# Kernel optimization log

Measured on AMD Instinct MI355X. Metric: run time of the kernel, lower is better.

## Reference

```python
import jax, jax.numpy as jnp
import numpy as np

SCALE = 256.0
QMIN, QMAX = -32768.0, 32767.0
EPS = 1e-5
NUM_HEADS = 16

def fpq(t):
    return jnp.clip(jnp.round(t * SCALE), QMIN, QMAX) / SCALE

def layer_norm(x, g, b):
    mu = jnp.mean(x, axis=-1, keepdims=True)
    var = jnp.mean(jnp.square(x - mu), axis=-1, keepdims=True)
    return (x - mu) * jax.lax.rsqrt(var + EPS) * g + b

def setup_inputs() -> dict:
    key = jax.random.key(0)
    ks = jax.random.split(key, 10)
    B, S, D, H = 8, 1024, 1024, 4096
    s = 1.0 / np.sqrt(D)
    sh = 1.0 / np.sqrt(H)
    return {
        "x": jax.random.normal(ks[0], (B, S, D), jnp.float32),
        "Wqkv": jax.random.uniform(ks[1], (D, 3 * D), jnp.float32, -s, s),
        "bqkv": jax.random.uniform(ks[2], (3 * D,), jnp.float32, -s, s),
        "Wout": jax.random.uniform(ks[3], (D, D), jnp.float32, -s, s),
        "bout": jax.random.uniform(ks[4], (D,), jnp.float32, -s, s),
        "W1": jax.random.uniform(ks[5], (D, H), jnp.float32, -s, s),
        "b1": jax.random.uniform(ks[6], (H,), jnp.float32, -s, s),
        "W2": jax.random.uniform(ks[7], (H, D), jnp.float32, -sh, sh),
        "b2": jax.random.uniform(ks[8], (D,), jnp.float32, -sh, sh),
        "g1": jnp.ones((D,), jnp.float32),
        "beta1": jnp.zeros((D,), jnp.float32),
        "g2": jnp.ones((D,), jnp.float32),
        "beta2": jnp.zeros((D,), jnp.float32),
    }

def reference(x, Wqkv, bqkv, Wout, bout, W1, b1, W2, b2, g1, beta1, g2, beta2):
    B, S, D = x.shape
    Hh = NUM_HEADS
    hd = D // Hh
    # --- attention on norm1(x) ---
    xn = layer_norm(x, g1, beta1)
    qkv = fpq(xn @ Wqkv + bqkv)                       # [B,S,3D]
    q, k, v = jnp.split(qkv, 3, axis=-1)
    q = q.reshape(B, S, Hh, hd).transpose(0, 2, 1, 3)  # [B,H,S,hd]
    k = k.reshape(B, S, Hh, hd).transpose(0, 2, 1, 3)
    v = v.reshape(B, S, Hh, hd).transpose(0, 2, 1, 3)
    scores = jnp.einsum("bhqd,bhkd->bhqk", q, k) / np.sqrt(hd)
    probs = fpq(jax.nn.softmax(scores, axis=-1))
    ctx = jnp.einsum("bhqk,bhkd->bhqd", probs, v)
    ctx = ctx.transpose(0, 2, 1, 3).reshape(B, S, D)
    attn = fpq(ctx @ Wout + bout)
    x = fpq(x + fpq(attn))
    # --- MLP on norm2(x) ---
    xn2 = layer_norm(x, g2, beta2)
    h = jax.nn.relu(fpq(xn2 @ W1 + b1))
    mlp = fpq(h @ W2 + b2)
    x = fpq(x + fpq(mlp))
    return x
```

## Files before the change

### kernel.cpp

```cpp
#include <hip/hip_runtime.h>
#include <hip/hip_fp16.h>
#include <stdint.h>

typedef _Float16 f16;
typedef _Float16 f16x4 __attribute__((ext_vector_type(4)));
typedef _Float16 f16x8 __attribute__((ext_vector_type(8)));
typedef float f32x4 __attribute__((ext_vector_type(4)));

__device__ __forceinline__ float fpq(float t) {
    float r = rintf(t * 256.0f);
    r = fminf(fmaxf(r, -32768.0f), 32767.0f);
    return r * 0.00390625f;
}

__device__ __forceinline__ int swzkey(int r) { return (r & 3) | ((r >> 1) & 4); }

__device__ __forceinline__ void gll16(const f16* g, f16* l) {
    __builtin_amdgcn_global_load_lds(
        (const __attribute__((address_space(1))) uint32_t*)g,
        (__attribute__((address_space(3))) uint32_t*)l, 16, 0, 0);
}

template <int N> __device__ __forceinline__ void waitvm() {
    if constexpr (N == 0)      asm volatile("s_waitcnt vmcnt(0)" ::: "memory");
    else if constexpr (N == 1) asm volatile("s_waitcnt vmcnt(1)" ::: "memory");
    else if constexpr (N == 2) asm volatile("s_waitcnt vmcnt(2)" ::: "memory");
    else if constexpr (N == 4) asm volatile("s_waitcnt vmcnt(4)" ::: "memory");
    else if constexpr (N == 6) asm volatile("s_waitcnt vmcnt(6)" ::: "memory");
    else                       asm volatile("s_waitcnt vmcnt(8)" ::: "memory");
}

__global__ __launch_bounds__(256) void ln_kernel(
        const float* __restrict__ x, const float* __restrict__ g,
        const float* __restrict__ b, f16* __restrict__ out) {
    int row = blockIdx.x;
    int t = threadIdx.x;
    const float4* xr = (const float4*)(x + (size_t)row * 1024);
    float4 v = xr[t];
    float s = v.x + v.y + v.z + v.w;
    float s2 = v.x * v.x + v.y * v.y + v.z * v.z + v.w * v.w;
#pragma unroll
    for (int o = 32; o >= 1; o >>= 1) {
        s += __shfl_down(s, o);
        s2 += __shfl_down(s2, o);
    }
    __shared__ float red[8];
    int wid = t >> 6;
    if ((t & 63) == 0) { red[wid] = s; red[4 + wid] = s2; }
    __syncthreads();
    float ts = red[0] + red[1] + red[2] + red[3];
    float ts2 = red[4] + red[5] + red[6] + red[7];
    float mu = ts * (1.0f / 1024.0f);
    float var = ts2 * (1.0f / 1024.0f) - mu * mu;
    float rs = rsqrtf(var + 1e-5f);
    float4 gg = ((const float4*)g)[t];
    float4 bb = ((const float4*)b)[t];
    f16x4 o4;
    o4[0] = (f16)((v.x - mu) * rs * gg.x + bb.x);
    o4[1] = (f16)((v.y - mu) * rs * gg.y + bb.y);
    o4[2] = (f16)((v.z - mu) * rs * gg.z + bb.z);
    o4[3] = (f16)((v.w - mu) * rs * gg.w + bb.w);
    ((f16x4*)out)[(size_t)row * 256 + t] = o4;
}

__global__ __launch_bounds__(256) void transpose_kernel(
        const float* __restrict__ W, f16* __restrict__ WT, int K, int N) {
    __shared__ float tile[32][33];
    int n0 = blockIdx.x * 32, k0 = blockIdx.y * 32;
    int tx = threadIdx.x & 31, ty = threadIdx.x >> 5;
#pragma unroll
    for (int i = 0; i < 32; i += 8)
        tile[ty + i][tx] = W[(size_t)(k0 + ty + i) * N + n0 + tx];
    __syncthreads();
#pragma unroll
    for (int i = 0; i < 32; i += 8)
        WT[(size_t)(n0 + ty + i) * K + k0 + tx] = (f16)tile[tx][ty + i];
}

template <int EPI>
__global__ __launch_bounds__(256, 2) void gemmd_kernel(
        const f16* __restrict__ A, const f16* __restrict__ BT,
        int N, int K, int GM, int GN,
        const float* __restrict__ bias, const float* __restrict__ resid,
        void* __restrict__ out0, f16* __restrict__ outk, f16* __restrict__ outv) {
    constexpr int ABUF = 128 * 64;
    constexpr int BUFSZ = 2 * ABUF;
    __shared__ f16 lds[2 * BUFSZ];

    int nwg = GM * GN;
    int orig = blockIdx.x;
    int wg = (orig & 7) * (nwg >> 3) + (orig >> 3);
    int st = wg >> 6, in = wg & 63;
    int bm = (st % (GM >> 3)) * 8 + (in >> 3);
    int bn = (st / (GM >> 3)) * 8 + (in & 7);
    int m0 = bm * 128, n0 = bn * 128;
    int tid = threadIdx.x;
    int lane = tid & 63;
    int lr = lane & 15, lg = lane >> 4;
    int wv = tid >> 6;
    int wm = wv >> 1, wn = wv & 1;

    size_t srcA[4], srcB[4]; int dst[4];
#pragma unroll
    for (int j = 0; j < 4; ++j) {
        int row = j * 32 + (tid >> 3);
        int slot = (tid & 7) ^ (row & 7);
        srcA[j] = (size_t)(m0 + row) * K + slot * 8;
        srcB[j] = (size_t)(n0 + row) * K + slot * 8;
        dst[j] = j * 2048 + tid * 8;
    }

    int offA[2][4], offB[4][2];
#pragma unroll
    for (int i = 0; i < 4; ++i) {
        int row = wm * 64 + i * 16 + lr;
#pragma unroll
        for (int kk = 0; kk < 2; ++kk)
            offA[kk][i] = row * 64 + (((kk * 4 + lg) ^ (row & 7)) * 8);
    }
#pragma unroll
    for (int j = 0; j < 4; ++j) {
        int n = wn * 64 + j * 16 + lr;
#pragma unroll
        for (int kk = 0; kk < 2; ++kk)
            offB[j][kk] = ABUF + n * 64 + (((kk * 4 + lg) ^ (n & 7)) * 8);
    }

    f32x4 acc[4][4] = {};
    int NT = K >> 6;

#pragma unroll
    for (int j = 0; j < 4; ++j) gll16(A + srcA[j], lds + dst[j]);
#pragma unroll
    for (int j = 0; j < 4; ++j) gll16(BT + srcB[j], lds + ABUF + dst[j]);
#pragma unroll
    for (int j = 0; j < 4; ++j) gll16(A + srcA[j] + 64, lds + BUFSZ + dst[j]);
#pragma unroll
    for (int j = 0; j < 4; ++j) gll16(BT + srcB[j] + 64, lds + BUFSZ + ABUF + dst[j]);
    waitvm<8>();
    __builtin_amdgcn_s_barrier();
    __builtin_amdgcn_sched_barrier(0);

    for (int t = 0; t < NT; ++t) {
        int cur = t & 1;
        f16* Ab = lds + cur * BUFSZ;
        f16x8 a0[4], a1[4], b00, b01, b10, b11;
#pragma unroll
        for (int i = 0; i < 4; ++i) a0[i] = *(const f16x8*)&Ab[offA[0][i]];
        b00 = *(const f16x8*)&Ab[offB[0][0]];
        b01 = *(const f16x8*)&Ab[offB[1][0]];
#pragma unroll
        for (int i = 0; i < 4; ++i) a1[i] = *(const f16x8*)&Ab[offA[1][i]];
        b10 = *(const f16x8*)&Ab[offB[0][1]];
        b11 = *(const f16x8*)&Ab[offB[1][1]];
        __builtin_amdgcn_s_setprio(1);
#pragma unroll
        for (int i = 0; i < 4; ++i) {
            acc[i][0] = __builtin_amdgcn_mfma_f32_16x16x32_f16(a0[i], b00, acc[i][0], 0, 0, 0);
            acc[i][1] = __builtin_amdgcn_mfma_f32_16x16x32_f16(a0[i], b01, acc[i][1], 0, 0, 0);
        }
#pragma unroll
        for (int i = 0; i < 4; ++i) {
            acc[i][0] = __builtin_amdgcn_mfma_f32_16x16x32_f16(a1[i], b10, acc[i][0], 0, 0, 0);
            acc[i][1] = __builtin_amdgcn_mfma_f32_16x16x32_f16(a1[i], b11, acc[i][1], 0, 0, 0);
        }
        __builtin_amdgcn_s_setprio(0);
        f16x8 b20 = *(const f16x8*)&Ab[offB[2][0]];
        f16x8 b30 = *(const f16x8*)&Ab[offB[3][0]];
        f16x8 b21 = *(const f16x8*)&Ab[offB[2][1]];
        f16x8 b31 = *(const f16x8*)&Ab[offB[3][1]];
        asm volatile("s_waitcnt lgkmcnt(0)" ::: "memory");
        __builtin_amdgcn_sched_barrier(0);
        __builtin_amdgcn_s_barrier();
        if (t + 2 < NT) {
            size_t kof = (size_t)(t + 2) << 6;
#pragma unroll
            for (int j = 0; j < 4; ++j) gll16(A + srcA[j] + kof, Ab + dst[j]);
#pragma unroll
            for (int j = 0; j < 4; ++j) gll16(BT + srcB[j] + kof, Ab + ABUF + dst[j]);
        }
        __builtin_amdgcn_s_setprio(1);
#pragma unroll
        for (int i = 0; i < 4; ++i) {
            acc[i][2] = __builtin_amdgcn_mfma_f32_16x16x32_f16(a0[i], b20, acc[i][2], 0, 0, 0);
            acc[i][3] = __builtin_amdgcn_mfma_f32_16x16x32_f16(a0[i], b30, acc[i][3], 0, 0, 0);
        }
#pragma unroll
        for (int i = 0; i < 4; ++i) {
            acc[i][2] = __builtin_amdgcn_mfma_f32_16x16x32_f16(a1[i], b21, acc[i][2], 0, 0, 0);
            acc[i][3] = __builtin_amdgcn_mfma_f32_16x16x32_f16(a1[i], b31, acc[i][3], 0, 0, 0);
        }
        __builtin_amdgcn_s_setprio(0);
        if (t + 2 < NT) { waitvm<8>(); }
        else if (t + 1 < NT) { waitvm<0>(); }
        __builtin_amdgcn_sched_barrier(0);
        __builtin_amdgcn_s_barrier();
    }

#pragma unroll
    for (int i = 0; i < 4; ++i) {
#pragma unroll
        for (int j = 0; j < 4; ++j) {
            int col = n0 + wn * 64 + j * 16 + lr;
            float bv = bias[col];
#pragma unroll
            for (int r = 0; r < 4; ++r) {
                int row = m0 + wm * 64 + i * 16 + lg * 4 + r;
                float val = acc[i][j][r] + bv;
                if (EPI == 0) {
                    float qv = fpq(val);
                    int part = col >> 10, wi = col & 1023;
                    int hd = wi >> 6, d = wi & 63;
                    int bb = row >> 10, ss = row & 1023;
                    size_t bh = (size_t)(bb * 16 + hd);
                    if (part == 0) {
                        ((f16*)out0)[(bh * 1024 + ss) * 64 + d] = (f16)qv;
                    } else if (part == 1) {
                        outk[bh * 65536 + (ss >> 6) * 4096 + (ss & 63) * 64 + (d ^ (swzkey(ss) << 3))] = (f16)qv;
                    } else {
                        outv[bh * 65536 + (ss >> 6) * 4096 + d * 64 + ((ss & 63) ^ (swzkey(d) << 3))] = (f16)qv;
                    }
                } else if (EPI == 2) {
                    float hv = fmaxf(fpq(val), 0.0f);
                    ((f16*)out0)[(size_t)row * N + col] = (f16)hv;
                } else {
                    float o = fpq(resid[(size_t)row * 1024 + col] + fpq(val));
                    ((float*)out0)[(size_t)row * 1024 + col] = o;
                }
            }
        }
    }
}

__global__ __launch_bounds__(512) void attn_kernel(
        const f16* __restrict__ Q, const f16* __restrict__ Kg,
        const f16* __restrict__ Vt, f16* __restrict__ ctx) {
    int id = blockIdx.x;
    int qt = (id >> 3) & 7;
    int bh = (id >> 6) * 8 + (id & 7);
    int b = bh >> 4, h = bh & 15;
    const f16* Qp = Q + ((size_t)bh * 1024 + (size_t)qt * 128) * 64;
    const f16* Kp = Kg + (size_t)bh * 65536;
    const f16* Vp = Vt + (size_t)bh * 65536;
    int t = threadIdx.x, lane = t & 63, w = t >> 6;
    int lr = lane & 15, lg = lane >> 4;
    __shared__ f16 Ks[2][4096];
    __shared__ f16 Vs[2][4096];
    int so = t * 8;

    const float L2E = 1.4426950408889634f;
    const float C0 = -24.0f * 1.4426950408889634f;

    f16x8 qf[2];
#pragma unroll
    for (int kk = 0; kk < 2; ++kk) {
        qf[kk] = *(const f16x8*)(Qp + (w * 16 + lr) * 64 + kk * 32 + lg * 8);
#pragma unroll
        for (int j = 0; j < 8; ++j) qf[kk][j] = qf[kk][j] * (f16)0.125f;
    }
    int koff[4][2], voff[4][2];
#pragma unroll
    for (int nf = 0; nf < 4; ++nf) {
        int rowv = 32 * (nf >> 1) + 8 * ((lr >> 2) ^ (2 * (nf & 1))) + 4 * (nf & 1) + (lr & 3);
#pragma unroll
        for (int kk = 0; kk < 2; ++kk)
            koff[nf][kk] = rowv * 64 + (((kk * 4 + lg) ^ swzkey(rowv)) * 8);
    }
#pragma unroll
    for (int db = 0; db < 4; ++db) {
        int d = db * 16 + lr;
#pragma unroll
        for (int kk = 0; kk < 2; ++kk)
            voff[db][kk] = d * 64 + (((kk * 4 + lg) ^ swzkey(d)) * 8);
    }

    gll16(Kp + so, Ks[0] + so);
    float lsum = 0.0f;
    for (int kt = 0; kt < 16; ++kt) {
        int cur = kt & 1;
        if (kt < 15) {
            gll16(Kp + (kt + 1) * 4096 + so, Ks[cur ^ 1] + so);
            waitvm<1>();
        } else {
            waitvm<0>();
        }
        __builtin_amdgcn_sched_barrier(0);
        __builtin_amdgcn_s_barrier();
        f32x4 sc[4] = {};
#pragma unroll
        for (int kk = 0; kk < 2; ++kk)
#pragma unroll
            for (int nf = 0; nf < 4; ++nf) {
                f16x8 kf = *(const f16x8*)&Ks[cur][koff[nf][kk]];
                sc[nf] = __builtin_amdgcn_mfma_f32_16x16x32_f16(kf, qf[kk], sc[nf], 0, 0, 0);
            }
        float part = 0.0f;
#pragma unroll
        for (int nf = 0; nf < 4; ++nf)
#pragma unroll
            for (int r = 0; r < 4; ++r)
                part += __builtin_amdgcn_exp2f(fmaf(sc[nf][r], L2E, C0));
        lsum += part;
        __builtin_amdgcn_s_barrier();
    }
    lsum += __shfl_xor(lsum, 16);
    lsum += __shfl_xor(lsum, 32);
    float rl256 = 256.0f * __builtin_amdgcn_rcpf(lsum);

    f32x4 co[4] = {};
    const float inv256 = 0.00390625f;
    gll16(Kp + so, Ks[0] + so);
    gll16(Vp + so, Vs[0] + so);
    for (int kt = 0; kt < 16; ++kt) {
        int cur = kt & 1;
        if (kt < 15) {
            gll16(Kp + (kt + 1) * 4096 + so, Ks[cur ^ 1] + so);
            gll16(Vp + (kt + 1) * 4096 + so, Vs[cur ^ 1] + so);
            waitvm<2>();
        } else {
            waitvm<0>();
        }
        __builtin_amdgcn_sched_barrier(0);
        __builtin_amdgcn_s_barrier();
        f32x4 sc[4] = {};
#pragma unroll
        for (int kk = 0; kk < 2; ++kk)
#pragma unroll
            for (int nf = 0; nf < 4; ++nf) {
                f16x8 kf = *(const f16x8*)&Ks[cur][koff[nf][kk]];
                sc[nf] = __builtin_amdgcn_mfma_f32_16x16x32_f16(kf, qf[kk], sc[nf], 0, 0, 0);
            }
        uint32_t pk0[4], pk1[4];
#pragma unroll
        for (int nf = 0; nf < 4; ++nf) {
            float e0 = __builtin_amdgcn_exp2f(fmaf(sc[nf][0], L2E, C0));
            float e1 = __builtin_amdgcn_exp2f(fmaf(sc[nf][1], L2E, C0));
            float e2 = __builtin_amdgcn_exp2f(fmaf(sc[nf][2], L2E, C0));
            float e3 = __builtin_amdgcn_exp2f(fmaf(sc[nf][3], L2E, C0));
            float r0 = rintf(e0 * rl256);
            float r1 = rintf(e1 * rl256);
            float r2 = rintf(e2 * rl256);
            float r3 = rintf(e3 * rl256);
            pk0[nf] = __builtin_bit_cast(uint32_t,
                        __builtin_amdgcn_cvt_pkrtz(r0 * inv256, r1 * inv256));
            pk1[nf] = __builtin_bit_cast(uint32_t,
                        __builtin_amdgcn_cvt_pkrtz(r2 * inv256, r3 * inv256));
        }
#pragma unroll
        for (int kk = 0; kk < 2; ++kk) {
            uint4 fw;
            fw.x = pk0[2 * kk];
            fw.y = pk1[2 * kk];
            fw.z = __shfl_xor(pk0[2 * kk + 1], 32);
            fw.w = __shfl_xor(pk1[2 * kk + 1], 32);
            f16x8 pa = __builtin_bit_cast(f16x8, fw);
#pragma unroll
            for (int db = 0; db < 4; ++db) {
                f16x8 vb = *(const f16x8*)&Vs[cur][voff[db][kk]];
                co[db] = __builtin_amdgcn_mfma_f32_16x16x32_f16(pa, vb, co[db], 0, 0, 0);
            }
        }
        __builtin_amdgcn_s_barrier();
    }
#pragma unroll
    for (int db = 0; db < 4; ++db)
#pragma unroll
        for (int r = 0; r < 4; ++r) {
            int ss = qt * 128 + w * 16 + lg * 4 + r;
            ctx[((size_t)b * 1024 + ss) * 1024 + h * 64 + db * 16 + lr] = (f16)co[db][r];
        }
}

extern "C" void kernel_launch(void* const* d_in, const int* in_sizes, int n_in,
                              void* d_out, int out_size, void* d_ws, size_t ws_size,
                              hipStream_t stream) {
    const float* x     = (const float*)d_in[0];
    const float* Wqkv  = (const float*)d_in[1];
    const float* bqkv  = (const float*)d_in[2];
    const float* Wout  = (const float*)d_in[3];
    const float* bout  = (const float*)d_in[4];
    const float* W1    = (const float*)d_in[5];
    const float* b1    = (const float*)d_in[6];
    const float* W2    = (const float*)d_in[7];
    const float* b2    = (const float*)d_in[8];
    const float* g1    = (const float*)d_in[9];
    const float* beta1 = (const float*)d_in[10];
    const float* g2    = (const float*)d_in[11];
    const float* beta2 = (const float*)d_in[12];

    char* ws = (char*)d_ws;
    const size_t MB = 1ull << 20;
    f16*  q_h   = (f16*)(ws);
    f16*  k_h   = (f16*)(ws + 16 * MB);
    f16*  vt_h  = (f16*)(ws + 32 * MB);
    f16*  ctx_h = (f16*)(ws + 48 * MB);
    f16*  h_h   = (f16*)(ws);
    f16*  xn_h  = (f16*)(ws + 64 * MB);
    float* x1   = (float*)(ws + 80 * MB);
    f16*  wT    = (f16*)(ws + 112 * MB);

    ln_kernel<<<8192, 256, 0, stream>>>(x, g1, beta1, xn_h);
    transpose_kernel<<<dim3(96, 32), 256, 0, stream>>>(Wqkv, wT, 1024, 3072);
    gemmd_kernel<0><<<1536, 256, 0, stream>>>(xn_h, wT, 3072, 1024, 64, 24, bqkv, nullptr, q_h, k_h, vt_h);
    attn_kernel<<<1024, 512, 0, stream>>>(q_h, k_h, vt_h, ctx_h);
    transpose_kernel<<<dim3(32, 32), 256, 0, stream>>>(Wout, wT, 1024, 1024);
    gemmd_kernel<1><<<512, 256, 0, stream>>>(ctx_h, wT, 1024, 1024, 64, 8, bout, x, x1, nullptr, nullptr);
    ln_kernel<<<8192, 256, 0, stream>>>(x1, g2, beta2, xn_h);
    transpose_kernel<<<dim3(128, 32), 256, 0, stream>>>(W1, wT, 1024, 4096);
    gemmd_kernel<2><<<2048, 256, 0, stream>>>(xn_h, wT, 4096, 1024, 64, 32, b1, nullptr, h_h, nullptr, nullptr);
    transpose_kernel<<<dim3(32, 128), 256, 0, stream>>>(W2, wT, 4096, 1024);
    gemmd_kernel<3><<<512, 256, 0, stream>>>(h_h, wT, 1024, 4096, 64, 8, b2, x1, d_out, nullptr, nullptr);
}
```

Measured before the change: 364.0 us.

## Halve GEMM K-tile to 32 and raise occupancy to four workgroups per CU

```diff
diff --git a/kernel.cpp b/kernel.cpp
--- a/kernel.cpp
+++ b/kernel.cpp
@@ -14,6 +14,7 @@
 }
 
 __device__ __forceinline__ int swzkey(int r) { return (r & 3) | ((r >> 1) & 4); }
+__device__ __forceinline__ int kk2(int r) { return (r >> 1) & 3; }
 
 __device__ __forceinline__ void gll16(const f16* g, f16* l) {
     __builtin_amdgcn_global_load_lds(
@@ -78,12 +79,12 @@
 }
 
 template <int EPI>
-__global__ __launch_bounds__(256, 2) void gemmd_kernel(
+__global__ __launch_bounds__(256, 4) void gemmd_kernel(
         const f16* __restrict__ A, const f16* __restrict__ BT,
         int N, int K, int GM, int GN,
         const float* __restrict__ bias, const float* __restrict__ resid,
         void* __restrict__ out0, f16* __restrict__ outk, f16* __restrict__ outv) {
-    constexpr int ABUF = 128 * 64;
+    constexpr int ABUF = 128 * 32;
     constexpr int BUFSZ = 2 * ABUF;
     __shared__ f16 lds[2 * BUFSZ];
 
@@ -100,98 +101,65 @@
     int wv = tid >> 6;
     int wm = wv >> 1, wn = wv & 1;
 
-    size_t srcA[4], srcB[4]; int dst[4];
-#pragma unroll
-    for (int j = 0; j < 4; ++j) {
-        int row = j * 32 + (tid >> 3);
-        int slot = (tid & 7) ^ (row & 7);
+    size_t srcA[2], srcB[2]; int dst[2];
+#pragma unroll
+    for (int j = 0; j < 2; ++j) {
+        int row = j * 64 + (tid >> 2);
+        int slot = (tid & 3) ^ kk2(row);
         srcA[j] = (size_t)(m0 + row) * K + slot * 8;
         srcB[j] = (size_t)(n0 + row) * K + slot * 8;
         dst[j] = j * 2048 + tid * 8;
     }
 
-    int offA[2][4], offB[4][2];
+    int offA[4], offB[4];
 #pragma unroll
     for (int i = 0; i < 4; ++i) {
         int row = wm * 64 + i * 16 + lr;
-#pragma unroll
-        for (int kk = 0; kk < 2; ++kk)
-            offA[kk][i] = row * 64 + (((kk * 4 + lg) ^ (row & 7)) * 8);
-    }
-#pragma unroll
-    for (int j = 0; j < 4; ++j) {
-        int n = wn * 64 + j * 16 + lr;
-#pragma unroll
-        for (int kk = 0; kk < 2; ++kk)
-            offB[j][kk] = ABUF + n * 64 + (((kk * 4 + lg) ^ (n & 7)) * 8);
+        offA[i] = row * 32 + ((lg ^ kk2(row)) * 8);
+        int n = wn * 64 + i * 16 + lr;
+        offB[i] = ABUF + n * 32 + ((lg ^ kk2(n)) * 8);
     }
 
     f32x4 acc[4][4] = {};
-    int NT = K >> 6;
-
-#pragma unroll
-    for (int j = 0; j < 4; ++j) gll16(A + srcA[j], lds + dst[j]);
-#pragma unroll
-    for (int j = 0; j < 4; ++j) gll16(BT + srcB[j], lds + ABUF + dst[j]);
-#pragma unroll
-    for (int j = 0; j < 4; ++j) gll16(A + srcA[j] + 64, lds + BUFSZ + dst[j]);
-#pragma unroll
-    for (int j = 0; j < 4; ++j) gll16(BT + srcB[j] + 64, lds + BUFSZ + ABUF + dst[j]);
-    waitvm<8>();
+    int NT = K >> 5;
+
+#pragma unroll
+    for (int j = 0; j < 2; ++j) gll16(A + srcA[j], lds + dst[j]);
+#pragma unroll
+    for (int j = 0; j < 2; ++j) gll16(BT + srcB[j], lds + ABUF + dst[j]);
+#pragma unroll
+    for (int j = 0; j < 2; ++j) gll16(A + srcA[j] + 32, lds + BUFSZ + dst[j]);
+#pragma unroll
+    for (int j = 0; j < 2; ++j) gll16(BT + srcB[j] + 32, lds + BUFSZ + ABUF + dst[j]);
+    waitvm<4>();
     __builtin_amdgcn_s_barrier();
     __builtin_amdgcn_sched_barrier(0);
 
     for (int t = 0; t < NT; ++t) {
-        int cur = t & 1;
-        f16* Ab = lds + cur * BUFSZ;
-        f16x8 a0[4], a1[4], b00, b01, b10, b11;
-#pragma unroll
-        for (int i = 0; i < 4; ++i) a0[i] = *(const f16x8*)&Ab[offA[0][i]];
-        b00 = *(const f16x8*)&Ab[offB[0][0]];
-        b01 = *(const f16x8*)&Ab[offB[1][0]];
-#pragma unroll
-        for (int i = 0; i < 4; ++i) a1[i] = *(const f16x8*)&Ab[offA[1][i]];
-        b10 = *(const f16x8*)&Ab[offB[0][1]];
-        b11 = *(const f16x8*)&Ab[offB[1][1]];
-        __builtin_amdgcn_s_setprio(1);
-#pragma unroll
-        for (int i = 0; i < 4; ++i) {
-            acc[i][0] = __builtin_amdgcn_mfma_f32_16x16x32_f16(a0[i], b00, acc[i][0], 0, 0, 0);
-            acc[i][1] = __builtin_amdgcn_mfma_f32_16x16x32_f16(a0[i], b01, acc[i][1], 0, 0, 0);
-        }
-#pragma unroll
-        for (int i = 0; i < 4; ++i) {
-            acc[i][0] = __builtin_amdgcn_mfma_f32_16x16x32_f16(a1[i], b10, acc[i][0], 0, 0, 0);
-            acc[i][1] = __builtin_amdgcn_mfma_f32_16x16x32_f16(a1[i], b11, acc[i][1], 0, 0, 0);
-        }
-        __builtin_amdgcn_s_setprio(0);
-        f16x8 b20 = *(const f16x8*)&Ab[offB[2][0]];
-        f16x8 b30 = *(const f16x8*)&Ab[offB[3][0]];
-        f16x8 b21 = *(const f16x8*)&Ab[offB[2][1]];
-        f16x8 b31 = *(const f16x8*)&Ab[offB[3][1]];
+        f16* Ab = lds + (t & 1) * BUFSZ;
+        f16x8 af[4], bf[4];
+#pragma unroll
+        for (int i = 0; i < 4; ++i) af[i] = *(const f16x8*)&Ab[offA[i]];
+#pragma unroll
+        for (int j = 0; j < 4; ++j) bf[j] = *(const f16x8*)&Ab[offB[j]];
         asm volatile("s_waitcnt lgkmcnt(0)" ::: "memory");
         __builtin_amdgcn_sched_barrier(0);
         __builtin_amdgcn_s_barrier();
         if (t + 2 < NT) {
-            size_t kof = (size_t)(t + 2) << 6;
-#pragma unroll
-            for (int j = 0; j < 4; ++j) gll16(A + srcA[j] + kof, Ab + dst[j]);
-#pragma unroll
-            for (int j = 0; j < 4; ++j) gll16(BT + srcB[j] + kof, Ab + ABUF + dst[j]);
+            size_t kof = (size_t)(t + 2) << 5;
+#pragma unroll
+            for (int j = 0; j < 2; ++j) gll16(A + srcA[j] + kof, Ab + dst[j]);
+#pragma unroll
+            for (int j = 0; j < 2; ++j) gll16(BT + srcB[j] + kof, Ab + ABUF + dst[j]);
         }
         __builtin_amdgcn_s_setprio(1);
 #pragma unroll
-        for (int i = 0; i < 4; ++i) {
-            acc[i][2] = __builtin_amdgcn_mfma_f32_16x16x32_f16(a0[i], b20, acc[i][2], 0, 0, 0);
-            acc[i][3] = __builtin_amdgcn_mfma_f32_16x16x32_f16(a0[i], b30, acc[i][3], 0, 0, 0);
-        }
-#pragma unroll
-        for (int i = 0; i < 4; ++i) {
-            acc[i][2] = __builtin_amdgcn_mfma_f32_16x16x32_f16(a1[i], b21, acc[i][2], 0, 0, 0);
-            acc[i][3] = __builtin_amdgcn_mfma_f32_16x16x32_f16(a1[i], b31, acc[i][3], 0, 0, 0);
-        }
+        for (int i = 0; i < 4; ++i)
+#pragma unroll
+            for (int j = 0; j < 4; ++j)
+                acc[i][j] = __builtin_amdgcn_mfma_f32_16x16x32_f16(af[i], bf[j], acc[i][j], 0, 0, 0);
         __builtin_amdgcn_s_setprio(0);
-        if (t + 2 < NT) { waitvm<8>(); }
+        if (t + 2 < NT) { waitvm<4>(); }
         else if (t + 1 < NT) { waitvm<0>(); }
         __builtin_amdgcn_sched_barrier(0);
         __builtin_amdgcn_s_barrier();
```

Result: slower. 389.1 us (+6.9%).
